# Performance work log

Hardware: AMD Instinct MI355X
Metric: run time of the kernel (lower is better)

The kernel has to match this reference:

```python
import jax, jax.numpy as jnp
import numpy as np

D_MODEL = 1024
H = 16
HEAD_DIM = D_MODEL // H  # 64


def setup_inputs() -> dict:
    key = jax.random.key(0)
    ks = jax.random.split(key, 11)
    B, S, D = 1, 4096, D_MODEL
    scale = 1.0 / np.sqrt(D)
    inp = {
        'q': jax.random.normal(ks[0], (B, S, D), jnp.float32),
        'k': jax.random.normal(ks[1], (B, S, D), jnp.float32),
        'v': jax.random.normal(ks[2], (B, S, D), jnp.float32),
        'w_q': jax.random.normal(ks[3], (D, D), jnp.float32) * scale,
        'b_q': jnp.zeros((D,), jnp.float32),
        'w_k': jax.random.normal(ks[4], (D, D), jnp.float32) * scale,
        'b_k': jnp.zeros((D,), jnp.float32),
        'w_v': jax.random.normal(ks[5], (D, D), jnp.float32) * scale,
        'b_v': jnp.zeros((D,), jnp.float32),
        'w_o': jax.random.normal(ks[6], (D, D), jnp.float32) * scale,
        'b_o': jnp.zeros((D,), jnp.float32),
    }
    return inp


def reference(q, k, v, w_q, b_q, w_k, b_k, w_v, b_v, w_o, b_o):
    B, Sq, D = q.shape
    Sk = k.shape[1]
    # Linear projections (torch Linear: x @ W.T + b), split into heads: [B,H,S,hd]
    Q = (q @ w_q.T + b_q).reshape(B, Sq, H, HEAD_DIM).transpose(0, 2, 1, 3)
    K = (k @ w_k.T + b_k).reshape(B, Sk, H, HEAD_DIM).transpose(0, 2, 1, 3)
    V = (v @ w_v.T + b_v).reshape(B, Sk, H, HEAD_DIM).transpose(0, 2, 1, 3)
    # Naive attention: full [B,H,Sq,Sk] scores, softmax, then AV
    scores = jnp.einsum('bhqd,bhkd->bhqk', Q, K) / jnp.sqrt(jnp.float32(HEAD_DIM))
    attn = jax.nn.softmax(scores, axis=-1)
    ctx = jnp.einsum('bhqk,bhkd->bhqd', attn, V)
    concat = ctx.transpose(0, 2, 1, 3).reshape(B, Sq, D)
    return concat @ w_o.T + b_o
```

## Files before the change

### kernel.cpp

```cpp
#include <hip/hip_runtime.h>
#include <stdint.h>

#define S_LEN 4096
#define DM 1024
#define NH 16

typedef __attribute__((ext_vector_type(8))) short short8;
typedef __attribute__((ext_vector_type(4))) float float4v;
typedef __attribute__((ext_vector_type(4))) unsigned short ushort4v;

typedef __attribute__((address_space(1))) const void* as1cvp;
typedef __attribute__((address_space(3))) void* as3vp;

#define MFMA16(a, b, c) __builtin_amdgcn_mfma_f32_16x16x32_bf16((a), (b), (c), 0, 0, 0)
#define GLOAD_LDS16(g, l) \
  __builtin_amdgcn_global_load_lds((as1cvp)(g), (as3vp)(l), 16, 0, 0)

__device__ __forceinline__ unsigned short f2bf(float f) {
  unsigned u = __float_as_uint(f);
  u += 0x7fffu + ((u >> 16) & 1u);
  return (unsigned short)(u >> 16);
}

__global__ __launch_bounds__(256) void cast_all(
    const float* __restrict__ q, const float* __restrict__ k, const float* __restrict__ v,
    const float* __restrict__ wq, const float* __restrict__ wk, const float* __restrict__ wv,
    const float* __restrict__ wo, unsigned short* __restrict__ dst)
{
  const float* src; size_t off; int n;
  switch (blockIdx.y) {
    case 0: src = q;  off = 0u;        n = 4194304; break;
    case 1: src = k;  off = 4194304u;  n = 4194304; break;
    case 2: src = v;  off = 8388608u;  n = 4194304; break;
    case 3: src = wq; off = 12582912u; n = 1048576; break;
    case 4: src = wk; off = 13631488u; n = 1048576; break;
    case 5: src = wv; off = 14680064u; n = 1048576; break;
    default: src = wo; off = 15728640u; n = 1048576; break;
  }
  int nv = n >> 2;
  for (int i = blockIdx.x * blockDim.x + threadIdx.x; i < nv; i += gridDim.x * blockDim.x) {
    float4v val = ((const float4v*)src)[i];
    ushort4v o;
    o.x = f2bf(val.x); o.y = f2bf(val.y); o.z = f2bf(val.z); o.w = f2bf(val.w);
    ((ushort4v*)(dst + off))[i] = o;
  }
}

template<int MODE>
__device__ __forceinline__ void gemm128(
    const unsigned short* __restrict__ A, const unsigned short* __restrict__ Bw,
    unsigned short* Cb, float* Cf, const float* __restrict__ bias, float alpha,
    unsigned short* As, unsigned short* Bs)
{
  const int K = 1024, N = 1024;
  int bm = blockIdx.x, bn = blockIdx.y;
  int t = threadIdx.x, lane = t & 63, w = t >> 6;
  int l15 = lane & 15, l4 = lane >> 4;
  int wr = w >> 1, wc = w & 1;

  float4v acc[4][4] = {};

  for (int kt = 0; kt < K / 32; ++kt) {
#pragma unroll
    for (int i = 0; i < 2; ++i) {
      int ci = i * 256 + t;
      int r = ci >> 2, cb = ci & 3;
      GLOAD_LDS16(A + (size_t)(bm * 128 + r) * K + kt * 32 + cb * 8,
                  As + (size_t)(i * 256 + w * 64) * 8);
      GLOAD_LDS16(Bw + (size_t)(bn * 128 + r) * K + kt * 32 + cb * 8,
                  Bs + (size_t)(i * 256 + w * 64) * 8);
    }
    __syncthreads();
    short8 af[4], bfr[4];
#pragma unroll
    for (int mf = 0; mf < 4; ++mf)
      af[mf] = *(const short8*)&As[(wr * 64 + mf * 16 + l15) * 32 + l4 * 8];
#pragma unroll
    for (int nf = 0; nf < 4; ++nf)
      bfr[nf] = *(const short8*)&Bs[(wc * 64 + nf * 16 + l15) * 32 + l4 * 8];
#pragma unroll
    for (int mf = 0; mf < 4; ++mf)
#pragma unroll
      for (int nf = 0; nf < 4; ++nf)
        acc[mf][nf] = MFMA16(af[mf], bfr[nf], acc[mf][nf]);
    __syncthreads();
  }

#pragma unroll
  for (int mf = 0; mf < 4; ++mf)
#pragma unroll
    for (int nf = 0; nf < 4; ++nf) {
      int col = bn * 128 + wc * 64 + nf * 16 + l15;
      float bv = bias[col];
#pragma unroll
      for (int j = 0; j < 4; ++j) {
        int row = bm * 128 + wr * 64 + mf * 16 + l4 * 4 + j;
        float val = (acc[mf][nf][j] + bv) * alpha;
        if (MODE == 1)      Cf[(size_t)row * N + col] = val;
        else if (MODE == 2) Cb[(size_t)col * S_LEN + row] = f2bf(val);
        else                Cb[(size_t)row * N + col] = f2bf(val);
      }
    }
}

__global__ __launch_bounds__(256) void proj_qkv(
    const unsigned short* xq, const unsigned short* xk, const unsigned short* xv,
    const unsigned short* wq, const unsigned short* wk, const unsigned short* wv,
    unsigned short* Qp, unsigned short* Kp, unsigned short* Vt,
    const float* bq, const float* bk, const float* bv)
{
  __shared__ unsigned short As[128 * 32], Bs[128 * 32];
  switch (blockIdx.z) {
    case 0:  gemm128<0>(xq, wq, Qp, nullptr, bq, 0.125f, As, Bs); break;
    case 1:  gemm128<0>(xk, wk, Kp, nullptr, bk, 1.0f,   As, Bs); break;
    default: gemm128<2>(xv, wv, Vt, nullptr, bv, 1.0f,   As, Bs); break;
  }
}

__global__ __launch_bounds__(256) void proj_o(
    const unsigned short* ctx, const unsigned short* wo, float* out, const float* bo)
{
  __shared__ unsigned short As[128 * 32], Bs[128 * 32];
  gemm128<1>(ctx, wo, nullptr, out, bo, 1.0f, As, Bs);
}

template<int BUF>
__device__ __forceinline__ void attn_tile(
    int kt,
    const unsigned short* kb0, const unsigned short* kb1,
    const unsigned short* vb0, const unsigned short* vb1,
    unsigned short* pw, const unsigned short* pr,
    const unsigned short* kg, const unsigned short* vg,
    unsigned short* kls, unsigned short* vls,
    const short8 (&qf)[2], float4v (&acc_o)[4], float& m_run, float& l_run,
    int l4)
{
  if (kt + 1 < 64) {
    GLOAD_LDS16(kg + (size_t)(kt + 1) * (64 * DM), kls + (1 - BUF) * 4096);
    GLOAD_LDS16(vg + (kt + 1) * 64, vls + (1 - BUF) * 4096);
  }

  float4v sc[4];
#pragma unroll
  for (int nf = 0; nf < 4; ++nf) {
    short8 kf0 = *(const short8*)(kb0 + BUF * 4096 + nf * 1024);
    short8 kf1 = *(const short8*)(kb1 + BUF * 4096 + nf * 1024);
    float4v z = {0.f, 0.f, 0.f, 0.f};
    z = MFMA16(kf0, qf[0], z);
    sc[nf] = MFMA16(kf1, qf[1], z);
  }

  float mx = fmaxf(fmaxf(fmaxf(sc[0][0], sc[0][1]), sc[0][2]), sc[0][3]);
#pragma unroll
  for (int nf = 1; nf < 4; ++nf)
    mx = fmaxf(fmaxf(fmaxf(fmaxf(mx, sc[nf][0]), sc[nf][1]), sc[nf][2]), sc[nf][3]);
  mx = fmaxf(mx, __shfl_xor(mx, 16));
  mx = fmaxf(mx, __shfl_xor(mx, 32));

  if (!__all(mx <= m_run + 8.f)) {
    float mnew = fmaxf(m_run, mx);
    float corr = __expf(m_run - mnew);
    m_run = mnew;
    l_run *= corr;
#pragma unroll
    for (int j = 0; j < 4; ++j) {
      float cj = __shfl(corr, l4 * 4 + j);
#pragma unroll
      for (int nf2 = 0; nf2 < 4; ++nf2) acc_o[nf2][j] *= cj;
    }
  }

  float ps = 0.f;
#pragma unroll
  for (int nf = 0; nf < 4; ++nf) {
    float p0 = __expf(sc[nf][0] - m_run);
    float p1 = __expf(sc[nf][1] - m_run);
    float p2 = __expf(sc[nf][2] - m_run);
    float p3 = __expf(sc[nf][3] - m_run);
    ps += (p0 + p1) + (p2 + p3);
    unsigned lo, hi;
    asm("v_cvt_pk_bf16_f32 %0, %1, %2" : "=v"(lo) : "v"(p0), "v"(p1));
    asm("v_cvt_pk_bf16_f32 %0, %1, %2" : "=v"(hi) : "v"(p2), "v"(p3));
    uint2 u; u.x = lo; u.y = hi;
    *(uint2*)(pw + nf * 16) = u;
  }
  ps += __shfl_xor(ps, 16);
  ps += __shfl_xor(ps, 32);
  l_run += ps;

  short8 pf[2];
#pragma unroll
  for (int kc = 0; kc < 2; ++kc)
    pf[kc] = *(const short8*)(pr + kc * 32);

#pragma unroll
  for (int nfd = 0; nfd < 4; ++nfd) {
    short8 vf0 = *(const short8*)(vb0 + BUF * 4096 + nfd * 1024);
    short8 vf1 = *(const short8*)(vb1 + BUF * 4096 + nfd * 1024);
    acc_o[nfd] = MFMA16(pf[0], vf0, acc_o[nfd]);
    acc_o[nfd] = MFMA16(pf[1], vf1, acc_o[nfd]);
  }
  __syncthreads();
}

__global__ __launch_bounds__(512) void attn_fused(
    const unsigned short* __restrict__ Qp, const unsigned short* __restrict__ Kp,
    const unsigned short* __restrict__ Vt, unsigned short* __restrict__ ctx)
{
  __shared__ unsigned short Ks[2][64 * 64];
  __shared__ unsigned short Vts[2][64 * 64];
  __shared__ unsigned short Ps[8][16 * 72];

  int bid = blockIdx.x;
  int wg = (bid & 7) * 64 + (bid >> 3);
  int h = wg >> 5, qt = wg & 31;

  int t = threadIdx.x, lane = t & 63, w = t >> 6;
  int l15 = lane & 15, l4 = lane >> 4;

  short8 qf[2];
  int qrow0 = qt * 128 + w * 16;
#pragma unroll
  for (int ks = 0; ks < 2; ++ks)
    qf[ks] = *(const short8*)&Qp[(size_t)(qrow0 + l15) * DM + h * 64 + ks * 32 + l4 * 8];

  float4v acc_o[4] = {};
  float m_run = -INFINITY, l_run = 0.f;

  const int swz = l15 & 7;
  const unsigned short* kb0 = &Ks[0][l15 * 64 + ((l4) ^ swz) * 8];
  const unsigned short* kb1 = &Ks[0][l15 * 64 + ((4 + l4) ^ swz) * 8];
  const unsigned short* vb0 = &Vts[0][l15 * 64 + ((l4) ^ swz) * 8];
  const unsigned short* vb1 = &Vts[0][l15 * 64 + ((4 + l4) ^ swz) * 8];
  unsigned short* pw = &Ps[w][l15 * 72 + l4 * 4];
  const unsigned short* pr = &Ps[w][l15 * 72 + l4 * 8];

  int sr = t >> 3, sp = t & 7;
  int slb = sp ^ (sr & 7);
  const unsigned short* kg = Kp + (size_t)sr * DM + h * 64 + slb * 8;
  const unsigned short* vg = Vt + (size_t)(h * 64 + sr) * S_LEN + slb * 8;
  unsigned short* kls = &Ks[0][t * 8];
  unsigned short* vls = &Vts[0][t * 8];

  GLOAD_LDS16(kg, kls);
  GLOAD_LDS16(vg, vls);
  __syncthreads();

  for (int kt = 0; kt < 64; kt += 2) {
    attn_tile<0>(kt,     kb0, kb1, vb0, vb1, pw, pr, kg, vg, kls, vls, qf, acc_o, m_run, l_run, l4);
    attn_tile<1>(kt + 1, kb0, kb1, vb0, vb1, pw, pr, kg, vg, kls, vls, qf, acc_o, m_run, l_run, l4);
  }

#pragma unroll
  for (int j = 0; j < 4; ++j) {
    float lj = __shfl(l_run, l4 * 4 + j);
    float inv = 1.0f / lj;
#pragma unroll
    for (int nfd = 0; nfd < 4; ++nfd) {
      int row = qrow0 + l4 * 4 + j;
      int col = h * 64 + nfd * 16 + l15;
      ctx[(size_t)row * DM + col] = f2bf(acc_o[nfd][j] * inv);
    }
  }
}

extern "C" void kernel_launch(void* const* d_in, const int* in_sizes, int n_in,
                              void* d_out, int out_size, void* d_ws, size_t ws_size,
                              hipStream_t stream) {
  const float* q  = (const float*)d_in[0];
  const float* k  = (const float*)d_in[1];
  const float* v  = (const float*)d_in[2];
  const float* wq = (const float*)d_in[3];
  const float* bq = (const float*)d_in[4];
  const float* wk = (const float*)d_in[5];
  const float* bk = (const float*)d_in[6];
  const float* wv = (const float*)d_in[7];
  const float* bv = (const float*)d_in[8];
  const float* wo = (const float*)d_in[9];
  const float* bo = (const float*)d_in[10];

  unsigned short* ws  = (unsigned short*)d_ws;
  unsigned short* qb  = ws;
  unsigned short* kb  = ws + 4194304u;
  unsigned short* vb  = ws + 8388608u;
  unsigned short* wqb = ws + 12582912u;
  unsigned short* wkb = ws + 13631488u;
  unsigned short* wvb = ws + 14680064u;
  unsigned short* wob = ws + 15728640u;
  unsigned short* Qp  = ws + 16777216u;
  unsigned short* Kp  = ws + 20971520u;
  unsigned short* Vt  = ws + 25165824u;
  unsigned short* ctx = qb;
  float* out = (float*)d_out;

  cast_all<<<dim3(1024, 7), 256, 0, stream>>>(q, k, v, wq, wk, wv, wo, ws);
  proj_qkv<<<dim3(32, 8, 3), 256, 0, stream>>>(qb, kb, vb, wqb, wkb, wvb, Qp, Kp, Vt, bq, bk, bv);
  attn_fused<<<dim3(512), 512, 0, stream>>>(Qp, Kp, Vt, ctx);
  proj_o<<<dim3(32, 8), 256, 0, stream>>>(ctx, wob, out, bo);
}
```

Baseline: 191.1 us.

## Process two 16-row query fragments per wave in attention with 256-thread blocks

The attention kernel now uses 4 waves per block instead of 8, and each wave handles 32 query rows as two 16-row MFMA fragments. Each K/V fragment read from LDS is reused for two MFMAs, which halves LDS read traffic per unit of compute and doubles instruction-level parallelism per wave. Each thread now issues two global-to-LDS loads per tile to fill the same 64x64 K/V tiles. The cost is higher register pressure from doubled accumulators and fewer waves per block, which may reduce occupancy and latency hiding.

```diff
diff --git a/kernel.cpp b/kernel.cpp
--- a/kernel.cpp
+++ b/kernel.cpp
@@ -132,84 +132,97 @@
     unsigned short* pw, const unsigned short* pr,
     const unsigned short* kg, const unsigned short* vg,
     unsigned short* kls, unsigned short* vls,
-    const short8 (&qf)[2], float4v (&acc_o)[4], float& m_run, float& l_run,
-    int l4)
+    const short8 (&qf)[2][2], float4v (&acc_o)[2][4],
+    float (&m_run)[2], float (&l_run)[2], int l4)
 {
   if (kt + 1 < 64) {
-    GLOAD_LDS16(kg + (size_t)(kt + 1) * (64 * DM), kls + (1 - BUF) * 4096);
-    GLOAD_LDS16(vg + (kt + 1) * 64, vls + (1 - BUF) * 4096);
-  }
-
-  float4v sc[4];
+    GLOAD_LDS16(kg + (size_t)(kt + 1) * (64 * DM),            kls + (1 - BUF) * 4096);
+    GLOAD_LDS16(kg + (size_t)(kt + 1) * (64 * DM) + 32 * DM,  kls + (1 - BUF) * 4096 + 2048);
+    GLOAD_LDS16(vg + (kt + 1) * 64,                           vls + (1 - BUF) * 4096);
+    GLOAD_LDS16(vg + (kt + 1) * 64 + 32 * S_LEN,              vls + (1 - BUF) * 4096 + 2048);
+  }
+
+  float4v sc[2][4];
 #pragma unroll
   for (int nf = 0; nf < 4; ++nf) {
     short8 kf0 = *(const short8*)(kb0 + BUF * 4096 + nf * 1024);
     short8 kf1 = *(const short8*)(kb1 + BUF * 4096 + nf * 1024);
-    float4v z = {0.f, 0.f, 0.f, 0.f};
-    z = MFMA16(kf0, qf[0], z);
-    sc[nf] = MFMA16(kf1, qf[1], z);
-  }
-
-  float mx = fmaxf(fmaxf(fmaxf(sc[0][0], sc[0][1]), sc[0][2]), sc[0][3]);
-#pragma unroll
-  for (int nf = 1; nf < 4; ++nf)
-    mx = fmaxf(fmaxf(fmaxf(fmaxf(mx, sc[nf][0]), sc[nf][1]), sc[nf][2]), sc[nf][3]);
-  mx = fmaxf(mx, __shfl_xor(mx, 16));
-  mx = fmaxf(mx, __shfl_xor(mx, 32));
-
-  if (!__all(mx <= m_run + 8.f)) {
-    float mnew = fmaxf(m_run, mx);
-    float corr = __expf(m_run - mnew);
-    m_run = mnew;
-    l_run *= corr;
-#pragma unroll
-    for (int j = 0; j < 4; ++j) {
-      float cj = __shfl(corr, l4 * 4 + j);
-#pragma unroll
-      for (int nf2 = 0; nf2 < 4; ++nf2) acc_o[nf2][j] *= cj;
-    }
-  }
-
-  float ps = 0.f;
-#pragma unroll
-  for (int nf = 0; nf < 4; ++nf) {
-    float p0 = __expf(sc[nf][0] - m_run);
-    float p1 = __expf(sc[nf][1] - m_run);
-    float p2 = __expf(sc[nf][2] - m_run);
-    float p3 = __expf(sc[nf][3] - m_run);
-    ps += (p0 + p1) + (p2 + p3);
-    unsigned lo, hi;
-    asm("v_cvt_pk_bf16_f32 %0, %1, %2" : "=v"(lo) : "v"(p0), "v"(p1));
-    asm("v_cvt_pk_bf16_f32 %0, %1, %2" : "=v"(hi) : "v"(p2), "v"(p3));
-    uint2 u; u.x = lo; u.y = hi;
-    *(uint2*)(pw + nf * 16) = u;
-  }
-  ps += __shfl_xor(ps, 16);
-  ps += __shfl_xor(ps, 32);
-  l_run += ps;
-
-  short8 pf[2];
-#pragma unroll
-  for (int kc = 0; kc < 2; ++kc)
-    pf[kc] = *(const short8*)(pr + kc * 32);
+#pragma unroll
+    for (int mf = 0; mf < 2; ++mf) {
+      float4v z = {0.f, 0.f, 0.f, 0.f};
+      z = MFMA16(kf0, qf[mf][0], z);
+      sc[mf][nf] = MFMA16(kf1, qf[mf][1], z);
+    }
+  }
+
+#pragma unroll
+  for (int mf = 0; mf < 2; ++mf) {
+    float mx = fmaxf(fmaxf(fmaxf(sc[mf][0][0], sc[mf][0][1]), sc[mf][0][2]), sc[mf][0][3]);
+#pragma unroll
+    for (int nf = 1; nf < 4; ++nf)
+      mx = fmaxf(fmaxf(fmaxf(fmaxf(mx, sc[mf][nf][0]), sc[mf][nf][1]), sc[mf][nf][2]), sc[mf][nf][3]);
+    mx = fmaxf(mx, __shfl_xor(mx, 16));
+    mx = fmaxf(mx, __shfl_xor(mx, 32));
+
+    if (!__all(mx <= m_run[mf] + 8.f)) {
+      float mnew = fmaxf(m_run[mf], mx);
+      float corr = __expf(m_run[mf] - mnew);
+      m_run[mf] = mnew;
+      l_run[mf] *= corr;
+#pragma unroll
+      for (int j = 0; j < 4; ++j) {
+        float cj = __shfl(corr, l4 * 4 + j);
+#pragma unroll
+        for (int nf2 = 0; nf2 < 4; ++nf2) acc_o[mf][nf2][j] *= cj;
+      }
+    }
+
+    float ps = 0.f;
+#pragma unroll
+    for (int nf = 0; nf < 4; ++nf) {
+      float p0 = __expf(sc[mf][nf][0] - m_run[mf]);
+      float p1 = __expf(sc[mf][nf][1] - m_run[mf]);
+      float p2 = __expf(sc[mf][nf][2] - m_run[mf]);
+      float p3 = __expf(sc[mf][nf][3] - m_run[mf]);
+      ps += (p0 + p1) + (p2 + p3);
+      unsigned lo, hi;
+      asm("v_cvt_pk_bf16_f32 %0, %1, %2" : "=v"(lo) : "v"(p0), "v"(p1));
+      asm("v_cvt_pk_bf16_f32 %0, %1, %2" : "=v"(hi) : "v"(p2), "v"(p3));
+      uint2 u; u.x = lo; u.y = hi;
+      *(uint2*)(pw + mf * 1152 + nf * 16) = u;
+    }
+    ps += __shfl_xor(ps, 16);
+    ps += __shfl_xor(ps, 32);
+    l_run[mf] += ps;
+  }
+
+  short8 pf[2][2];
+#pragma unroll
+  for (int mf = 0; mf < 2; ++mf)
+#pragma unroll
+    for (int kc = 0; kc < 2; ++kc)
+      pf[mf][kc] = *(const short8*)(pr + mf * 1152 + kc * 32);
 
 #pragma unroll
   for (int nfd = 0; nfd < 4; ++nfd) {
     short8 vf0 = *(const short8*)(vb0 + BUF * 4096 + nfd * 1024);
     short8 vf1 = *(const short8*)(vb1 + BUF * 4096 + nfd * 1024);
-    acc_o[nfd] = MFMA16(pf[0], vf0, acc_o[nfd]);
-    acc_o[nfd] = MFMA16(pf[1], vf1, acc_o[nfd]);
+#pragma unroll
+    for (int mf = 0; mf < 2; ++mf) {
+      acc_o[mf][nfd] = MFMA16(pf[mf][0], vf0, acc_o[mf][nfd]);
+      acc_o[mf][nfd] = MFMA16(pf[mf][1], vf1, acc_o[mf][nfd]);
+    }
   }
   __syncthreads();
 }
 
-__global__ __launch_bounds__(512) void attn_fused(
+__global__ __launch_bounds__(256) void attn_fused(
     const unsigned short* __restrict__ Qp, const unsigned short* __restrict__ Kp,
     const unsigned short* __restrict__ Vt, unsigned short* __restrict__ ctx)
 {
   __shared__ unsigned short Ks[2][64 * 64];
   __shared__ unsigned short Vts[2][64 * 64];
-  __shared__ unsigned short Ps[8][16 * 72];
+  __shared__ unsigned short Ps[4][32 * 72];
 
   int bid = blockIdx.x;
   int wg = (bid & 7) * 64 + (bid >> 3);
@@ -218,14 +231,17 @@
   int t = threadIdx.x, lane = t & 63, w = t >> 6;
   int l15 = lane & 15, l4 = lane >> 4;
 
-  short8 qf[2];
-  int qrow0 = qt * 128 + w * 16;
-#pragma unroll
-  for (int ks = 0; ks < 2; ++ks)
-    qf[ks] = *(const short8*)&Qp[(size_t)(qrow0 + l15) * DM + h * 64 + ks * 32 + l4 * 8];
-
-  float4v acc_o[4] = {};
-  float m_run = -INFINITY, l_run = 0.f;
+  short8 qf[2][2];
+  int qrow0 = qt * 128 + w * 32;
+#pragma unroll
+  for (int mf = 0; mf < 2; ++mf)
+#pragma unroll
+    for (int ks = 0; ks < 2; ++ks)
+      qf[mf][ks] = *(const short8*)&Qp[(size_t)(qrow0 + mf * 16 + l15) * DM + h * 64 + ks * 32 + l4 * 8];
+
+  float4v acc_o[2][4] = {};
+  float m_run[2] = {-INFINITY, -INFINITY};
+  float l_run[2] = {0.f, 0.f};
 
   const int swz = l15 & 7;
   const unsigned short* kb0 = &Ks[0][l15 * 64 + ((l4) ^ swz) * 8];
@@ -242,8 +258,10 @@
   unsigned short* kls = &Ks[0][t * 8];
   unsigned short* vls = &Vts[0][t * 8];
 
-  GLOAD_LDS16(kg, kls);
-  GLOAD_LDS16(vg, vls);
+  GLOAD_LDS16(kg,                kls);
+  GLOAD_LDS16(kg + 32 * DM,      kls + 2048);
+  GLOAD_LDS16(vg,                vls);
+  GLOAD_LDS16(vg + 32 * S_LEN,   vls + 2048);
   __syncthreads();
 
   for (int kt = 0; kt < 64; kt += 2) {
@@ -252,14 +270,17 @@
   }
 
 #pragma unroll
-  for (int j = 0; j < 4; ++j) {
-    float lj = __shfl(l_run, l4 * 4 + j);
-    float inv = 1.0f / lj;
-#pragma unroll
-    for (int nfd = 0; nfd < 4; ++nfd) {
-      int row = qrow0 + l4 * 4 + j;
-      int col = h * 64 + nfd * 16 + l15;
-      ctx[(size_t)row * DM + col] = f2bf(acc_o[nfd][j] * inv);
+  for (int mf = 0; mf < 2; ++mf) {
+#pragma unroll
+    for (int j = 0; j < 4; ++j) {
+      float lj = __shfl(l_run[mf], l4 * 4 + j);
+      float inv = 1.0f / lj;
+#pragma unroll
+      for (int nfd = 0; nfd < 4; ++nfd) {
+        int row = qrow0 + mf * 16 + l4 * 4 + j;
+        int col = h * 64 + nfd * 16 + l15;
+        ctx[(size_t)row * DM + col] = f2bf(acc_o[mf][nfd][j] * inv);
+      }
     }
   }
 }
@@ -295,6 +316,6 @@
 
   cast_all<<<dim3(1024, 7), 256, 0, stream>>>(q, k, v, wq, wk, wv, wo, ws);
   proj_qkv<<<dim3(32, 8, 3), 256, 0, stream>>>(qb, kb, vb, wqb, wkb, wvb, Qp, Kp, Vt, bq, bk, bv);
-  attn_fused<<<dim3(512), 512, 0, stream>>>(Qp, Kp, Vt, ctx);
+  attn_fused<<<dim3(512), 256, 0, stream>>>(Qp, Kp, Vt, ctx);
   proj_o<<<dim3(32, 8), 256, 0, stream>>>(ctx, wob, out, bo);
 }
```

Measured after the change: 201.2 us. 1.05x slower.

## Keep softmax probabilities in registers and use exp2 with folded log2e scale

Applied to the files above, without the earlier changes.

The P tile is no longer round-tripped through shared memory. Probabilities computed in the S-tile register layout are packed straight into A operands for 16x16x16 bf16 MFMAs, with V reads re-indexed to match. Separately, log2(e) is folded into the Q projection scale so the softmax can use the hardware v_exp_f32 (exp2) directly, and the rescale threshold is adjusted to match. The trade-off is twice as many smaller MFMAs and narrower V loads in exchange for removing the LDS writes and reads of P.

```diff
diff --git a/kernel.cpp b/kernel.cpp
--- a/kernel.cpp
+++ b/kernel.cpp
@@ -6,6 +6,7 @@
 #define NH 16
 
 typedef __attribute__((ext_vector_type(8))) short short8;
+typedef __attribute__((ext_vector_type(4))) short short4v;
 typedef __attribute__((ext_vector_type(4))) float float4v;
 typedef __attribute__((ext_vector_type(4))) unsigned short ushort4v;
 
@@ -13,6 +14,7 @@
 typedef __attribute__((address_space(3))) void* as3vp;
 
 #define MFMA16(a, b, c) __builtin_amdgcn_mfma_f32_16x16x32_bf16((a), (b), (c), 0, 0, 0)
+#define MFMA16K16(a, b, c) __builtin_amdgcn_mfma_f32_16x16x16bf16_1k((a), (b), (c), 0, 0, 0)
 #define GLOAD_LDS16(g, l) \
   __builtin_amdgcn_global_load_lds((as1cvp)(g), (as3vp)(l), 16, 0, 0)
 
@@ -20,6 +22,12 @@
   unsigned u = __float_as_uint(f);
   u += 0x7fffu + ((u >> 16) & 1u);
   return (unsigned short)(u >> 16);
+}
+
+__device__ __forceinline__ float exp2_hw(float x) {
+  float r;
+  asm("v_exp_f32 %0, %1" : "=v"(r) : "v"(x));
+  return r;
 }
 
 __global__ __launch_bounds__(256) void cast_all(
@@ -111,9 +119,9 @@
 {
   __shared__ unsigned short As[128 * 32], Bs[128 * 32];
   switch (blockIdx.z) {
-    case 0:  gemm128<0>(xq, wq, Qp, nullptr, bq, 0.125f, As, Bs); break;
-    case 1:  gemm128<0>(xk, wk, Kp, nullptr, bk, 1.0f,   As, Bs); break;
-    default: gemm128<2>(xv, wv, Vt, nullptr, bv, 1.0f,   As, Bs); break;
+    case 0:  gemm128<0>(xq, wq, Qp, nullptr, bq, 0.1803368867f, As, Bs); break;
+    case 1:  gemm128<0>(xk, wk, Kp, nullptr, bk, 1.0f,          As, Bs); break;
+    default: gemm128<2>(xv, wv, Vt, nullptr, bv, 1.0f,          As, Bs); break;
   }
 }
 
@@ -128,8 +136,7 @@
 __device__ __forceinline__ void attn_tile(
     int kt,
     const unsigned short* kb0, const unsigned short* kb1,
-    const unsigned short* vb0, const unsigned short* vb1,
-    unsigned short* pw, const unsigned short* pr,
+    const int (&vAe)[4], const unsigned short* vbase,
     const unsigned short* kg, const unsigned short* vg,
     unsigned short* kls, unsigned short* vls,
     const short8 (&qf)[2], float4v (&acc_o)[4], float& m_run, float& l_run,
@@ -157,9 +164,9 @@
   mx = fmaxf(mx, __shfl_xor(mx, 16));
   mx = fmaxf(mx, __shfl_xor(mx, 32));
 
-  if (!__all(mx <= m_run + 8.f)) {
+  if (!__all(mx <= m_run + 11.5f)) {
     float mnew = fmaxf(m_run, mx);
-    float corr = __expf(m_run - mnew);
+    float corr = exp2_hw(m_run - mnew);
     m_run = mnew;
     l_run *= corr;
 #pragma unroll
@@ -171,35 +178,33 @@
   }
 
   float ps = 0.f;
+  short4v pa[4];
 #pragma unroll
   for (int nf = 0; nf < 4; ++nf) {
-    float p0 = __expf(sc[nf][0] - m_run);
-    float p1 = __expf(sc[nf][1] - m_run);
-    float p2 = __expf(sc[nf][2] - m_run);
-    float p3 = __expf(sc[nf][3] - m_run);
+    float p0 = exp2_hw(sc[nf][0] - m_run);
+    float p1 = exp2_hw(sc[nf][1] - m_run);
+    float p2 = exp2_hw(sc[nf][2] - m_run);
+    float p3 = exp2_hw(sc[nf][3] - m_run);
     ps += (p0 + p1) + (p2 + p3);
     unsigned lo, hi;
     asm("v_cvt_pk_bf16_f32 %0, %1, %2" : "=v"(lo) : "v"(p0), "v"(p1));
     asm("v_cvt_pk_bf16_f32 %0, %1, %2" : "=v"(hi) : "v"(p2), "v"(p3));
-    uint2 u; u.x = lo; u.y = hi;
-    *(uint2*)(pw + nf * 16) = u;
+    union { unsigned u[2]; short4v s; } pk;
+    pk.u[0] = lo; pk.u[1] = hi;
+    pa[nf] = pk.s;
   }
   ps += __shfl_xor(ps, 16);
   ps += __shfl_xor(ps, 32);
   l_run += ps;
 
-  short8 pf[2];
-#pragma unroll
-  for (int kc = 0; kc < 2; ++kc)
-    pf[kc] = *(const short8*)(pr + kc * 32);
-
-#pragma unroll
-  for (int nfd = 0; nfd < 4; ++nfd) {
-    short8 vf0 = *(const short8*)(vb0 + BUF * 4096 + nfd * 1024);
-    short8 vf1 = *(const short8*)(vb1 + BUF * 4096 + nfd * 1024);
-    acc_o[nfd] = MFMA16(pf[0], vf0, acc_o[nfd]);
-    acc_o[nfd] = MFMA16(pf[1], vf1, acc_o[nfd]);
-  }
+#pragma unroll
+  for (int nfd = 0; nfd < 4; ++nfd)
+#pragma unroll
+    for (int nf = 0; nf < 4; ++nf) {
+      short4v vf = *(const short4v*)(vbase + vAe[nf] + BUF * 4096 + nfd * 1024);
+      acc_o[nfd] = MFMA16K16(pa[nf], vf, acc_o[nfd]);
+    }
+
   __syncthreads();
 }
 
@@ -209,7 +214,6 @@
 {
   __shared__ unsigned short Ks[2][64 * 64];
   __shared__ unsigned short Vts[2][64 * 64];
-  __shared__ unsigned short Ps[8][16 * 72];
 
   int bid = blockIdx.x;
   int wg = (bid & 7) * 64 + (bid >> 3);
@@ -230,10 +234,11 @@
   const int swz = l15 & 7;
   const unsigned short* kb0 = &Ks[0][l15 * 64 + ((l4) ^ swz) * 8];
   const unsigned short* kb1 = &Ks[0][l15 * 64 + ((4 + l4) ^ swz) * 8];
-  const unsigned short* vb0 = &Vts[0][l15 * 64 + ((l4) ^ swz) * 8];
-  const unsigned short* vb1 = &Vts[0][l15 * 64 + ((4 + l4) ^ swz) * 8];
-  unsigned short* pw = &Ps[w][l15 * 72 + l4 * 4];
-  const unsigned short* pr = &Ps[w][l15 * 72 + l4 * 8];
+  int vAe[4];
+#pragma unroll
+  for (int nf = 0; nf < 4; ++nf)
+    vAe[nf] = l15 * 64 + (((2 * nf + (l4 >> 1)) ^ swz) * 8) + (l4 & 1) * 4;
+  const unsigned short* vbase = &Vts[0][0];
 
   int sr = t >> 3, sp = t & 7;
   int slb = sp ^ (sr & 7);
@@ -247,8 +252,8 @@
   __syncthreads();
 
   for (int kt = 0; kt < 64; kt += 2) {
-    attn_tile<0>(kt,     kb0, kb1, vb0, vb1, pw, pr, kg, vg, kls, vls, qf, acc_o, m_run, l_run, l4);
-    attn_tile<1>(kt + 1, kb0, kb1, vb0, vb1, pw, pr, kg, vg, kls, vls, qf, acc_o, m_run, l_run, l4);
+    attn_tile<0>(kt,     kb0, kb1, vAe, vbase, kg, vg, kls, vls, qf, acc_o, m_run, l_run, l4);
+    attn_tile<1>(kt + 1, kb0, kb1, vAe, vbase, kg, vg, kls, vls, qf, acc_o, m_run, l_run, l4);
   }
 
 #pragma unroll
```

Measured after the change: 195.4 us. 2.2% more time.
